# Kernel tuning notes

Hardware: AMD Instinct MI355X
Metric: run time of the kernel (lower is better)

The kernel has to match this reference:

```python
import jax, jax.numpy as jnp
import numpy as np

MAX_DISP = 4  # init kwarg


def setup_inputs() -> dict:
    key = jax.random.key(0)
    k1, k2 = jax.random.split(key)
    x_1 = jax.random.normal(k1, (8, 128, 128, 128), dtype=jnp.float32)
    x_2 = jax.random.normal(k2, (8, 128, 128, 128), dtype=jnp.float32)
    return {"x_1": x_1, "x_2": x_2}


def reference(x_1, x_2):
    d = MAX_DISP
    H, W = x_1.shape[2], x_1.shape[3]
    # zero-pad x_2 by max_disp on both spatial dims (ConstantPad2d)
    x2p = jnp.pad(x_2, ((0, 0), (0, 0), (d, d), (d, d)))
    # loop over the fixed (2d+1)^2 = 81 displacement offsets (structural, not data dim)
    outs = [
        jnp.mean(x_1 * x2p[:, :, dx:dx + H, dy:dy + W], axis=1)  # [B,H,W]
        for dx in range(2 * d + 1)
        for dy in range(2 * d + 1)
    ]
    return jnp.stack(outs, axis=1)  # [B, 81, H, W]
```

## Files before the change

### kernel.cpp

```cpp
#include <hip/hip_runtime.h>


constexpr int Bn = 8, Cn = 128, Hn = 128, Wn = 128;
constexpr int HWn = Hn * Wn;

__device__ __forceinline__ float dpp_from_lower(float x) {
  return __int_as_float(
      __builtin_amdgcn_update_dpp(0, __float_as_int(x), 0x111, 0xF, 0xF, true));
}
__device__ __forceinline__ float dpp_from_upper(float x) {
  return __int_as_float(
      __builtin_amdgcn_update_dpp(0, __float_as_int(x), 0x101, 0xF, 0xF, true));
}

__global__ __launch_bounds__(64, 3)
void corr_kernel(const float* __restrict__ x1, const float* __restrict__ x2,
                 float* __restrict__ out) {
  const int lane = threadIdx.x;
  const int j    = lane & 15;
  const int px0  = j << 3;

  const int phys = blockIdx.x;
  const int b    = phys & 7;
  const int s    = phys >> 3;
  int rowl, dh;
  if (s < 256) {
    const int g = s >> 6;
    const int t = s & 63;
    rowl = (t << 1) + ((lane >> 4) & 1);
    dh   = (g << 1) - 4 + (lane >> 5);
  } else {
    const int t = s - 256;
    rowl = (t << 2) + (lane >> 4);
    dh   = 4;
  }
  const int x2row = rowl + dh;
  const bool ok = ((unsigned)x2row < (unsigned)Hn);

  const float* x1p = x1 + (size_t)b * Cn * HWn + rowl * Wn + px0;
  const float* x2p = x2 + (size_t)b * Cn * HWn + x2row * Wn + px0;

  float4 acc[9][2];
#pragma unroll
  for (int dw = 0; dw < 9; ++dw) {
    acc[dw][0] = make_float4(0.f, 0.f, 0.f, 0.f);
    acc[dw][1] = make_float4(0.f, 0.f, 0.f, 0.f);
  }

  const float4 fz = make_float4(0.f, 0.f, 0.f, 0.f);
  float4 A[2][2], B[2][2];
#pragma unroll
  for (int p = 0; p < 2; ++p) {
    const float* xp = x1p + (size_t)p * HWn;
    A[p][0] = *(const float4*)xp;
    A[p][1] = *(const float4*)(xp + 4);
    float4 t0 = fz, t1 = fz;
    if (ok) {
      const float* yp = x2p + (size_t)p * HWn;
      t0 = *(const float4*)yp;
      t1 = *(const float4*)(yp + 4);
    }
    B[p][0] = t0;
    B[p][1] = t1;
  }
  const float* pf1 = x1p + 2 * (size_t)HWn;
  const float* pf2 = x2p + 2 * (size_t)HWn;

#pragma unroll 2
  for (int cc = 0; cc < 128; ++cc) {
    const int sl = cc & 1;
    const float4 a0 = A[sl][0], a1 = A[sl][1];
    const float4 b0 = B[sl][0], b1 = B[sl][1];
    if (cc < 126) {
      A[sl][0] = *(const float4*)pf1;
      A[sl][1] = *(const float4*)(pf1 + 4);
      float4 t0 = fz, t1 = fz;
      if (ok) {
        t0 = *(const float4*)pf2;
        t1 = *(const float4*)(pf2 + 4);
      }
      B[sl][0] = t0;
      B[sl][1] = t1;
      pf1 += HWn;
      pf2 += HWn;
    }
    const float p4 = dpp_from_lower(b1.x);
    const float p5 = dpp_from_lower(b1.y);
    const float p6 = dpp_from_lower(b1.z);
    const float p7 = dpp_from_lower(b1.w);
    const float n0 = dpp_from_upper(b0.x);
    const float n1 = dpp_from_upper(b0.y);
    const float n2 = dpp_from_upper(b0.z);
    const float n3 = dpp_from_upper(b0.w);
    const float win[16] = {p4, p5, p6, p7, b0.x, b0.y, b0.z, b0.w,
                           b1.x, b1.y, b1.z, b1.w, n0, n1, n2, n3};
    const float av[8] = {a0.x, a0.y, a0.z, a0.w, a1.x, a1.y, a1.z, a1.w};
#pragma unroll
    for (int dw = 0; dw < 9; ++dw) {
      acc[dw][0].x += av[0] * win[dw + 0];
      acc[dw][0].y += av[1] * win[dw + 1];
      acc[dw][0].z += av[2] * win[dw + 2];
      acc[dw][0].w += av[3] * win[dw + 3];
      acc[dw][1].x += av[4] * win[dw + 4];
      acc[dw][1].y += av[5] * win[dw + 5];
      acc[dw][1].z += av[6] * win[dw + 6];
      acc[dw][1].w += av[7] * win[dw + 7];
    }
  }

  const float scale = 1.0f / 128.0f;
  const int obase = (dh + 4) * 9;
  float* ob = out + ((size_t)b * 81 + obase) * HWn + (size_t)rowl * Wn + px0;
#pragma unroll
  for (int dw = 0; dw < 9; ++dw) {
    float4 lo = acc[dw][0], hi = acc[dw][1];
    lo.x *= scale; lo.y *= scale; lo.z *= scale; lo.w *= scale;
    hi.x *= scale; hi.y *= scale; hi.z *= scale; hi.w *= scale;
    *(float4*)(ob + (size_t)dw * HWn)     = lo;
    *(float4*)(ob + (size_t)dw * HWn + 4) = hi;
  }
}

extern "C" void kernel_launch(void* const* d_in, const int* in_sizes, int n_in,
                              void* d_out, int out_size, void* d_ws, size_t ws_size,
                              hipStream_t stream) {
  const float* x1 = (const float*)d_in[0];
  const float* x2 = (const float*)d_in[1];
  float* out = (float*)d_out;
  const int n_wgs = Bn * (4 * 64 + 32);
  corr_kernel<<<dim3(n_wgs), dim3(64), 0, stream>>>(x1, x2, out);
}
```

Measured before the change: 193.2 us.

## Shrink per-lane tile to 4 pixels and shift neighbours with wave-wide DPP

```diff
diff --git a/kernel.cpp b/kernel.cpp
--- a/kernel.cpp
+++ b/kernel.cpp
@@ -4,64 +4,48 @@
 constexpr int Bn = 8, Cn = 128, Hn = 128, Wn = 128;
 constexpr int HWn = Hn * Wn;
 
-__device__ __forceinline__ float dpp_from_lower(float x) {
+__device__ __forceinline__ float wave_shr1(float x) {
   return __int_as_float(
-      __builtin_amdgcn_update_dpp(0, __float_as_int(x), 0x111, 0xF, 0xF, true));
+      __builtin_amdgcn_update_dpp(0, __float_as_int(x), 0x138, 0xF, 0xF, true));
 }
-__device__ __forceinline__ float dpp_from_upper(float x) {
+__device__ __forceinline__ float wave_shl1(float x) {
   return __int_as_float(
-      __builtin_amdgcn_update_dpp(0, __float_as_int(x), 0x101, 0xF, 0xF, true));
+      __builtin_amdgcn_update_dpp(0, __float_as_int(x), 0x130, 0xF, 0xF, true));
 }
 
-__global__ __launch_bounds__(64, 3)
+__global__ __launch_bounds__(64, 5)
 void corr_kernel(const float* __restrict__ x1, const float* __restrict__ x2,
                  float* __restrict__ out) {
   const int lane = threadIdx.x;
-  const int j    = lane & 15;
-  const int px0  = j << 3;
+  const int half = lane >> 5;
+  const int j    = lane & 31;
+  const int px0  = j << 2;
 
   const int phys = blockIdx.x;
   const int b    = phys & 7;
   const int s    = phys >> 3;
-  int rowl, dh;
-  if (s < 256) {
-    const int g = s >> 6;
-    const int t = s & 63;
-    rowl = (t << 1) + ((lane >> 4) & 1);
-    dh   = (g << 1) - 4 + (lane >> 5);
-  } else {
-    const int t = s - 256;
-    rowl = (t << 2) + (lane >> 4);
-    dh   = 4;
-  }
+  const int dh   = s % 9 - 4;
+  const int rowl = (s / 9) * 2 + half;
   const int x2row = rowl + dh;
   const bool ok = ((unsigned)x2row < (unsigned)Hn);
+  const bool jlo = (j == 0);
+  const bool jhi = (j == 31);
 
   const float* x1p = x1 + (size_t)b * Cn * HWn + rowl * Wn + px0;
   const float* x2p = x2 + (size_t)b * Cn * HWn + x2row * Wn + px0;
 
-  float4 acc[9][2];
+  float4 acc[9];
 #pragma unroll
-  for (int dw = 0; dw < 9; ++dw) {
-    acc[dw][0] = make_float4(0.f, 0.f, 0.f, 0.f);
-    acc[dw][1] = make_float4(0.f, 0.f, 0.f, 0.f);
-  }
+  for (int dw = 0; dw < 9; ++dw) acc[dw] = make_float4(0.f, 0.f, 0.f, 0.f);
 
   const float4 fz = make_float4(0.f, 0.f, 0.f, 0.f);
-  float4 A[2][2], B[2][2];
+  float4 A[2], B[2];
 #pragma unroll
   for (int p = 0; p < 2; ++p) {
-    const float* xp = x1p + (size_t)p * HWn;
-    A[p][0] = *(const float4*)xp;
-    A[p][1] = *(const float4*)(xp + 4);
-    float4 t0 = fz, t1 = fz;
-    if (ok) {
-      const float* yp = x2p + (size_t)p * HWn;
-      t0 = *(const float4*)yp;
-      t1 = *(const float4*)(yp + 4);
-    }
-    B[p][0] = t0;
-    B[p][1] = t1;
+    A[p] = *(const float4*)(x1p + (size_t)p * HWn);
+    float4 t = fz;
+    if (ok) t = *(const float4*)(x2p + (size_t)p * HWn);
+    B[p] = t;
   }
   const float* pf1 = x1p + 2 * (size_t)HWn;
   const float* pf2 = x2p + 2 * (size_t)HWn;
@@ -69,42 +53,36 @@
 #pragma unroll 2
   for (int cc = 0; cc < 128; ++cc) {
     const int sl = cc & 1;
-    const float4 a0 = A[sl][0], a1 = A[sl][1];
-    const float4 b0 = B[sl][0], b1 = B[sl][1];
+    const float4 a  = A[sl];
+    const float4 b0 = B[sl];
     if (cc < 126) {
-      A[sl][0] = *(const float4*)pf1;
-      A[sl][1] = *(const float4*)(pf1 + 4);
-      float4 t0 = fz, t1 = fz;
-      if (ok) {
-        t0 = *(const float4*)pf2;
-        t1 = *(const float4*)(pf2 + 4);
-      }
-      B[sl][0] = t0;
-      B[sl][1] = t1;
+      A[sl] = *(const float4*)pf1;
+      float4 t = fz;
+      if (ok) t = *(const float4*)pf2;
+      B[sl] = t;
       pf1 += HWn;
       pf2 += HWn;
     }
-    const float p4 = dpp_from_lower(b1.x);
-    const float p5 = dpp_from_lower(b1.y);
-    const float p6 = dpp_from_lower(b1.z);
-    const float p7 = dpp_from_lower(b1.w);
-    const float n0 = dpp_from_upper(b0.x);
-    const float n1 = dpp_from_upper(b0.y);
-    const float n2 = dpp_from_upper(b0.z);
-    const float n3 = dpp_from_upper(b0.w);
-    const float win[16] = {p4, p5, p6, p7, b0.x, b0.y, b0.z, b0.w,
-                           b1.x, b1.y, b1.z, b1.w, n0, n1, n2, n3};
-    const float av[8] = {a0.x, a0.y, a0.z, a0.w, a1.x, a1.y, a1.z, a1.w};
+    float p0 = wave_shr1(b0.x);
+    float p1 = wave_shr1(b0.y);
+    float p2 = wave_shr1(b0.z);
+    float p3 = wave_shr1(b0.w);
+    float n0 = wave_shl1(b0.x);
+    float n1 = wave_shl1(b0.y);
+    float n2 = wave_shl1(b0.z);
+    float n3 = wave_shl1(b0.w);
+    p0 = jlo ? 0.f : p0;  p1 = jlo ? 0.f : p1;
+    p2 = jlo ? 0.f : p2;  p3 = jlo ? 0.f : p3;
+    n0 = jhi ? 0.f : n0;  n1 = jhi ? 0.f : n1;
+    n2 = jhi ? 0.f : n2;  n3 = jhi ? 0.f : n3;
+    const float win[12] = {p0, p1, p2, p3, b0.x, b0.y, b0.z, b0.w,
+                           n0, n1, n2, n3};
 #pragma unroll
     for (int dw = 0; dw < 9; ++dw) {
-      acc[dw][0].x += av[0] * win[dw + 0];
-      acc[dw][0].y += av[1] * win[dw + 1];
-      acc[dw][0].z += av[2] * win[dw + 2];
-      acc[dw][0].w += av[3] * win[dw + 3];
-      acc[dw][1].x += av[4] * win[dw + 4];
-      acc[dw][1].y += av[5] * win[dw + 5];
-      acc[dw][1].z += av[6] * win[dw + 6];
-      acc[dw][1].w += av[7] * win[dw + 7];
+      acc[dw].x += a.x * win[dw + 0];
+      acc[dw].y += a.y * win[dw + 1];
+      acc[dw].z += a.z * win[dw + 2];
+      acc[dw].w += a.w * win[dw + 3];
     }
   }
 
@@ -113,11 +91,9 @@
   float* ob = out + ((size_t)b * 81 + obase) * HWn + (size_t)rowl * Wn + px0;
 #pragma unroll
   for (int dw = 0; dw < 9; ++dw) {
-    float4 lo = acc[dw][0], hi = acc[dw][1];
-    lo.x *= scale; lo.y *= scale; lo.z *= scale; lo.w *= scale;
-    hi.x *= scale; hi.y *= scale; hi.z *= scale; hi.w *= scale;
-    *(float4*)(ob + (size_t)dw * HWn)     = lo;
-    *(float4*)(ob + (size_t)dw * HWn + 4) = hi;
+    float4 v = acc[dw];
+    v.x *= scale; v.y *= scale; v.z *= scale; v.w *= scale;
+    *(float4*)(ob + (size_t)dw * HWn) = v;
   }
 }
 
@@ -127,6 +103,6 @@
   const float* x1 = (const float*)d_in[0];
   const float* x2 = (const float*)d_in[1];
   float* out = (float*)d_out;
-  const int n_wgs = Bn * (4 * 64 + 32);
+  const int n_wgs = Bn * 9 * (Hn / 2);
   corr_kernel<<<dim3(n_wgs), dim3(64), 0, stream>>>(x1, x2, out);
 }
```

Result: slower. 219.6 us (+13.7%).
